# Kernel optimization log

Measured on AMD Instinct MI355X. Metric: run time of the kernel, lower is better.

## Reference

```python
import jax, jax.numpy as jnp
import numpy as np

N_NODES = 50000
N_EDGES = 800000
IN_DIM = 256
HID = 128
OUT = 128
LEAKY_SLOPE = 0.01


def setup_inputs() -> dict:
    key = jax.random.key(0)
    ks = jax.random.split(key, 12)
    s = 0.05
    return {
        "h": jax.random.normal(ks[0], (N_NODES, IN_DIM), dtype=jnp.float32),
        "src": jax.random.randint(ks[1], (N_EDGES,), 0, N_NODES, dtype=jnp.int32),
        "dst": jax.random.randint(ks[2], (N_EDGES,), 0, N_NODES, dtype=jnp.int32),
        "W1": jax.random.normal(ks[3], (HID, IN_DIM), dtype=jnp.float32) * s,
        "b1": jax.random.normal(ks[4], (HID,), dtype=jnp.float32) * s,
        "a1": jax.random.normal(ks[5], (2 * HID,), dtype=jnp.float32) * s,
        "ab1": jax.random.normal(ks[6], (), dtype=jnp.float32) * s,
        "W2": jax.random.normal(ks[7], (OUT, HID), dtype=jnp.float32) * s,
        "b2": jax.random.normal(ks[8], (OUT,), dtype=jnp.float32) * s,
        "a2": jax.random.normal(ks[9], (2 * OUT,), dtype=jnp.float32) * s,
        "ab2": jax.random.normal(ks[10], (), dtype=jnp.float32) * s,
    }


def gat_layer(h, src, dst, W, b, a, ab, n_nodes):
    # z = fc(h)
    z = h @ W.T + b                      # [N, D]
    D = z.shape[-1]
    zs = z[src]                           # [E, D] gather src features
    zd = z[dst]                           # [E, D] gather dst features
    # attn_fc(cat[zs, zd]) == zs @ a[:D] + zd @ a[D:] + ab
    e = zs @ a[:D] + zd @ a[D:] + ab      # [E]
    e = jnp.where(e > 0, e, LEAKY_SLOPE * e)  # leaky_relu, slope 0.01
    # segment softmax over edges grouped by destination node
    m = jax.ops.segment_max(e, dst, num_segments=n_nodes)   # [N]
    ex = jnp.exp(e - m[dst])                                  # [E]
    denom = jax.ops.segment_sum(ex, dst, num_segments=n_nodes)  # [N]
    alpha = ex / denom[dst]                                   # [E]
    # weighted scatter-sum of src features into dst nodes
    return jax.ops.segment_sum(alpha[:, None] * zs, dst, num_segments=n_nodes)


def reference(h, src, dst, W1, b1, a1, ab1, W2, b2, a2, ab2):
    n = h.shape[0]
    h1 = jax.nn.elu(gat_layer(h, src, dst, W1, b1, a1, ab1, n))
    h2 = jax.nn.elu(gat_layer(h1, src, dst, W2, b2, a2, ab2, n))
    return h2
```

## Files before the change

kernel.cpp:

```cpp
#include <hip/hip_runtime.h>
#include <hip/hip_bf16.h>

#define N_NODES 50000
#define N_EDGES 800000
#define IN_DIM  256
#define HID     128
#define LEAKY   0.01f

#define EDGE_BLOCKS  ((N_EDGES + 255) / 256)
#define NODE_WBLKS   (N_NODES / 4)
#define SCAN_BLOCKS  ((N_NODES + 255) / 256)
#define MTILES       ((N_NODES + 31) / 32)
#define GEMM_WAVES   (MTILES * 2)
#define GEMM_BLOCKS  ((GEMM_WAVES + 3) / 4)

typedef __attribute__((ext_vector_type(8))) short short8;
typedef __attribute__((ext_vector_type(4))) float f32x4;

__device__ __forceinline__ unsigned short f2bf(float x) {
    union { __hip_bfloat16 b; unsigned short u; } c;
    c.b = __float2bfloat16(x);
    return c.u;
}
__device__ __forceinline__ float bf2f(unsigned short u) {
    union { unsigned int u; float f; } c;
    c.u = ((unsigned int)u) << 16;
    return c.f;
}
__device__ __forceinline__ float2 bfu2(unsigned int u) {
    float2 r;
    r.x = bf2f((unsigned short)(u & 0xffff));
    r.y = bf2f((unsigned short)(u >> 16));
    return r;
}
__device__ __forceinline__ float lky(float x) { return x > 0.f ? x : LEAKY * x; }


__global__ void hist_split(const int* __restrict__ dst, int* __restrict__ counts,
                           const float* __restrict__ W1, unsigned short* __restrict__ w1hi,
                           unsigned short* __restrict__ w1lo,
                           const float* __restrict__ W2, unsigned short* __restrict__ w2hi,
                           unsigned short* __restrict__ w2lo) {
    int i = blockIdx.x * 256 + threadIdx.x;
    if (i < N_EDGES) atomicAdd(&counts[dst[i]], 1);
    if (i < HID * IN_DIM) {
        float x = W1[i];
        unsigned short h = f2bf(x);
        w1hi[i] = h;
        w1lo[i] = f2bf(x - bf2f(h));
    } else if (i < HID * IN_DIM + HID * HID) {
        int j = i - HID * IN_DIM;
        float x = W2[j];
        unsigned short h = f2bf(x);
        w2hi[j] = h;
        w2lo[j] = f2bf(x - bf2f(h));
    }
}

__global__ void scan_block(const int* __restrict__ counts, int* __restrict__ offsets,
                           int* __restrict__ bsums) {
    __shared__ int sh[256];
    int tid = threadIdx.x;
    int i = blockIdx.x * 256 + tid;
    int v = (i < N_NODES) ? counts[i] : 0;
    sh[tid] = v;
    __syncthreads();
    for (int o = 1; o < 256; o <<= 1) {
        int t = (tid >= o) ? sh[tid - o] : 0;
        __syncthreads();
        sh[tid] += t;
        __syncthreads();
    }
    if (i < N_NODES) offsets[i] = sh[tid] - v;
    if (tid == 255) bsums[blockIdx.x] = sh[255];
}

__global__ void scan_add(int* __restrict__ offsets, const int* __restrict__ bsums) {
    __shared__ int sh[256];
    int tid = threadIdx.x;
    int b = blockIdx.x;
    sh[tid] = (tid < b) ? bsums[tid] : 0;
    __syncthreads();
    for (int o = 128; o > 0; o >>= 1) {
        if (tid < o) sh[tid] += sh[tid + o];
        __syncthreads();
    }
    int base = sh[0];
    int i = b * 256 + tid;
    if (i < N_NODES) offsets[i] += base;
    if (i == N_NODES) offsets[N_NODES] = N_EDGES;
}

__global__ void fill_kernel(const int* __restrict__ dst, const int* __restrict__ src,
                            const int* __restrict__ offsets,
                            int* __restrict__ cursor, int* __restrict__ csr_src) {
    int i = blockIdx.x * 256 + threadIdx.x;
    if (i < N_EDGES) {
        int d = dst[i];
        int p = atomicAdd(&cursor[d], 1);
        csr_src[offsets[d] + p] = src[i];
    }
}


__device__ __forceinline__ void gemm_epilogue(
        const f32x4* acc, int m0, int q, int lane,
        const float* __restrict__ bias, const float* __restrict__ attn,
        unsigned short* __restrict__ Zb, float* __restrict__ sS, float* __restrict__ sD) {
    int r = lane & 15;
    int rowbase = m0 + (lane >> 4) * 4;
    float ps[4] = {0.f, 0.f, 0.f, 0.f};
    float pd[4] = {0.f, 0.f, 0.f, 0.f};
#pragma unroll
    for (int nt = 0; nt < 4; nt++) {
        int n = q * 64 + nt * 16 + r;
        float bn = bias[n];
        float aS = attn[n];
        float aD = attn[HID + n];
#pragma unroll
        for (int reg = 0; reg < 4; reg++) {
            float zv = acc[nt][reg] + bn;
            Zb[(size_t)(rowbase + reg) * HID + n] = f2bf(zv);
            ps[reg] += zv * aS;
            pd[reg] += zv * aD;
        }
    }
#pragma unroll
    for (int o = 1; o < 16; o <<= 1) {
#pragma unroll
        for (int reg = 0; reg < 4; reg++) {
            ps[reg] += __shfl_xor(ps[reg], o, 64);
            pd[reg] += __shfl_xor(pd[reg], o, 64);
        }
    }
    if (r == 0) {
#pragma unroll
        for (int reg = 0; reg < 4; reg++) {
            sS[q * N_NODES + rowbase + reg] = ps[reg];
            sD[q * N_NODES + rowbase + reg] = pd[reg];
        }
    }
}


__launch_bounds__(256)
__global__ void gemm_fc1(const float* __restrict__ A,
                         const unsigned short* __restrict__ Whi,
                         const unsigned short* __restrict__ Wlo,
                         const float* __restrict__ bias,
                         const float* __restrict__ attn,
                         unsigned short* __restrict__ Zb,
                         float* __restrict__ sS, float* __restrict__ sD) {
    int wave = blockIdx.x * 4 + (threadIdx.x >> 6);
    if (wave >= GEMM_WAVES) return;
    int lane = threadIdx.x & 63;
    int mt = wave >> 1;
    int q  = wave & 1;
    int m0 = mt * 32;
    bool has2 = (m0 + 16 < N_NODES);
    int r  = lane & 15;
    int ko = (lane >> 4) * 8;

    const float* Ap0 = A + (size_t)(m0 + r) * IN_DIM + ko;
    const float* Ap1 = has2 ? (Ap0 + 16 * IN_DIM) : Ap0;
    const unsigned short* Wh = Whi + (size_t)(q * 64 + r) * IN_DIM + ko;
    const unsigned short* Wl = Wlo + (size_t)(q * 64 + r) * IN_DIM + ko;

    f32x4 acc0[4], acc1[4];
#pragma unroll
    for (int i = 0; i < 4; i++) {
        acc0[i] = (f32x4){0.f, 0.f, 0.f, 0.f};
        acc1[i] = (f32x4){0.f, 0.f, 0.f, 0.f};
    }

    float4 c00 = *(const float4*)(Ap0);
    float4 c01 = *(const float4*)(Ap0 + 4);
    float4 c10 = *(const float4*)(Ap1);
    float4 c11 = *(const float4*)(Ap1 + 4);

#pragma unroll
    for (int kt = 0; kt < IN_DIM / 32; kt++) {
        float4 n00, n01, n10, n11;
        if (kt < IN_DIM / 32 - 1) {
            n00 = *(const float4*)(Ap0 + (kt + 1) * 32);
            n01 = *(const float4*)(Ap0 + (kt + 1) * 32 + 4);
            n10 = *(const float4*)(Ap1 + (kt + 1) * 32);
            n11 = *(const float4*)(Ap1 + (kt + 1) * 32 + 4);
        }
        float x0[8] = {c00.x, c00.y, c00.z, c00.w, c01.x, c01.y, c01.z, c01.w};
        float x1[8] = {c10.x, c10.y, c10.z, c10.w, c11.x, c11.y, c11.z, c11.w};
        short8 ahi0, alo0, ahi1, alo1;
#pragma unroll
        for (int j = 0; j < 8; j++) {
            unsigned short h0 = f2bf(x0[j]);
            ahi0[j] = (short)h0;
            alo0[j] = (short)f2bf(x0[j] - bf2f(h0));
            unsigned short h1 = f2bf(x1[j]);
            ahi1[j] = (short)h1;
            alo1[j] = (short)f2bf(x1[j] - bf2f(h1));
        }
#pragma unroll
        for (int nt = 0; nt < 4; nt++) {
            short8 bhi = *(const short8*)(Wh + (size_t)nt * 16 * IN_DIM + kt * 32);
            short8 blo = *(const short8*)(Wl + (size_t)nt * 16 * IN_DIM + kt * 32);
            acc0[nt] = __builtin_amdgcn_mfma_f32_16x16x32_bf16(ahi0, bhi, acc0[nt], 0, 0, 0);
            acc0[nt] = __builtin_amdgcn_mfma_f32_16x16x32_bf16(alo0, bhi, acc0[nt], 0, 0, 0);
            acc0[nt] = __builtin_amdgcn_mfma_f32_16x16x32_bf16(ahi0, blo, acc0[nt], 0, 0, 0);
            acc1[nt] = __builtin_amdgcn_mfma_f32_16x16x32_bf16(ahi1, bhi, acc1[nt], 0, 0, 0);
            acc1[nt] = __builtin_amdgcn_mfma_f32_16x16x32_bf16(alo1, bhi, acc1[nt], 0, 0, 0);
            acc1[nt] = __builtin_amdgcn_mfma_f32_16x16x32_bf16(ahi1, blo, acc1[nt], 0, 0, 0);
        }
        if (kt < IN_DIM / 32 - 1) { c00 = n00; c01 = n01; c10 = n10; c11 = n11; }
    }
    gemm_epilogue(acc0, m0, q, lane, bias, attn, Zb, sS, sD);
    if (has2) gemm_epilogue(acc1, m0 + 16, q, lane, bias, attn, Zb, sS, sD);
}


__launch_bounds__(256)
__global__ void gemm_fc2(const unsigned short* __restrict__ Abf,
                         const unsigned short* __restrict__ Whi,
                         const unsigned short* __restrict__ Wlo,
                         const float* __restrict__ bias,
                         const float* __restrict__ attn,
                         unsigned short* __restrict__ Zb,
                         float* __restrict__ sS, float* __restrict__ sD) {
    int wave = blockIdx.x * 4 + (threadIdx.x >> 6);
    if (wave >= GEMM_WAVES) return;
    int lane = threadIdx.x & 63;
    int mt = wave >> 1;
    int q  = wave & 1;
    int m0 = mt * 32;
    bool has2 = (m0 + 16 < N_NODES);
    int r  = lane & 15;
    int ko = (lane >> 4) * 8;

    const unsigned short* Ap0 = Abf + (size_t)(m0 + r) * HID + ko;
    const unsigned short* Ap1 = has2 ? (Ap0 + 16 * HID) : Ap0;
    const unsigned short* Wh = Whi + (size_t)(q * 64 + r) * HID + ko;
    const unsigned short* Wl = Wlo + (size_t)(q * 64 + r) * HID + ko;

    f32x4 acc0[4], acc1[4];
#pragma unroll
    for (int i = 0; i < 4; i++) {
        acc0[i] = (f32x4){0.f, 0.f, 0.f, 0.f};
        acc1[i] = (f32x4){0.f, 0.f, 0.f, 0.f};
    }

    short8 a0 = *(const short8*)(Ap0);
    short8 a1 = *(const short8*)(Ap1);

#pragma unroll
    for (int kt = 0; kt < HID / 32; kt++) {
        short8 na0, na1;
        if (kt < HID / 32 - 1) {
            na0 = *(const short8*)(Ap0 + (kt + 1) * 32);
            na1 = *(const short8*)(Ap1 + (kt + 1) * 32);
        }
#pragma unroll
        for (int nt = 0; nt < 4; nt++) {
            short8 bhi = *(const short8*)(Wh + (size_t)nt * 16 * HID + kt * 32);
            short8 blo = *(const short8*)(Wl + (size_t)nt * 16 * HID + kt * 32);
            acc0[nt] = __builtin_amdgcn_mfma_f32_16x16x32_bf16(a0, bhi, acc0[nt], 0, 0, 0);
            acc0[nt] = __builtin_amdgcn_mfma_f32_16x16x32_bf16(a0, blo, acc0[nt], 0, 0, 0);
            acc1[nt] = __builtin_amdgcn_mfma_f32_16x16x32_bf16(a1, bhi, acc1[nt], 0, 0, 0);
            acc1[nt] = __builtin_amdgcn_mfma_f32_16x16x32_bf16(a1, blo, acc1[nt], 0, 0, 0);
        }
        if (kt < HID / 32 - 1) { a0 = na0; a1 = na1; }
    }
    gemm_epilogue(acc0, m0, q, lane, bias, attn, Zb, sS, sD);
    if (has2) gemm_epilogue(acc1, m0 + 16, q, lane, bias, attn, Zb, sS, sD);
}


template <int OUT_BF>
__launch_bounds__(256)
__global__ void aggregate(const unsigned short* __restrict__ Zb,
                          const int* __restrict__ csr_src,
                          const int* __restrict__ offsets,
                          const float* __restrict__ sS,
                          const float* __restrict__ sD,
                          const float* __restrict__ ab,
                          unsigned short* __restrict__ OutBf,
                          float* __restrict__ OutF) {
    int v = blockIdx.x * 4 + (threadIdx.x >> 6);
    int lane = threadIdx.x & 63;
    int off = offsets[v];
    int deg = offsets[v + 1] - off;
    float sdv = sD[v] + sD[v + N_NODES] + ab[0];

    const unsigned int* Zrow = (const unsigned int*)Zb;
    float2 acc = {0.f, 0.f};

    if (deg <= 64) {
        bool act = lane < deg;
        int s_l = 0;
        float x = -3.0e38f;
        if (act) {
            s_l = csr_src[off + lane];
            x = lky(sS[s_l] + sS[s_l + N_NODES] + sdv);
        }
        float mx = x;
#pragma unroll
        for (int o = 32; o > 0; o >>= 1) mx = fmaxf(mx, __shfl_xor(mx, o, 64));
        float ex = act ? __expf(x - mx) : 0.f;
        float sum = ex;
#pragma unroll
        for (int o = 32; o > 0; o >>= 1) sum += __shfl_xor(sum, o, 64);
        float al_l = (deg > 0) ? ex / sum : 0.f;

        int t = 0;
        for (; t + 8 <= deg; t += 8) {
            int   s[8];
            float a[8];
            unsigned int rw[8];
#pragma unroll
            for (int j = 0; j < 8; j++) {
                s[j] = __shfl(s_l, t + j, 64);
                a[j] = __shfl(al_l, t + j, 64);
            }
#pragma unroll
            for (int j = 0; j < 8; j++)
                rw[j] = Zrow[(size_t)s[j] * (HID / 2) + lane];
#pragma unroll
            for (int j = 0; j < 8; j++) {
                float2 zz = bfu2(rw[j]);
                acc.x += a[j] * zz.x;
                acc.y += a[j] * zz.y;
            }
        }
        for (; t < deg; t++) {
            int sj = __shfl(s_l, t, 64);
            float aj = __shfl(al_l, t, 64);
            float2 zz = bfu2(Zrow[(size_t)sj * (HID / 2) + lane]);
            acc.x += aj * zz.x;
            acc.y += aj * zz.y;
        }
    } else {
        float mx = -3.0e38f;
        for (int t = lane; t < deg; t += 64) {
            int s = csr_src[off + t];
            mx = fmaxf(mx, lky(sS[s] + sS[s + N_NODES] + sdv));
        }
#pragma unroll
        for (int o = 32; o > 0; o >>= 1) mx = fmaxf(mx, __shfl_xor(mx, o, 64));
        float sum = 0.f;
        for (int t = lane; t < deg; t += 64) {
            int s = csr_src[off + t];
            sum += __expf(lky(sS[s] + sS[s + N_NODES] + sdv) - mx);
        }
#pragma unroll
        for (int o = 32; o > 0; o >>= 1) sum += __shfl_xor(sum, o, 64);
        float inv = 1.f / sum;
        for (int t = 0; t < deg; t++) {
            int s = csr_src[off + t];
            float al = __expf(lky(sS[s] + sS[s + N_NODES] + sdv) - mx) * inv;
            float2 zz = bfu2(Zrow[(size_t)s * (HID / 2) + lane]);
            acc.x += al * zz.x;
            acc.y += al * zz.y;
        }
    }

    acc.x = acc.x > 0.f ? acc.x : __expf(acc.x) - 1.f;
    acc.y = acc.y > 0.f ? acc.y : __expf(acc.y) - 1.f;

    if (OUT_BF) {
        ushort2 o2;
        o2.x = f2bf(acc.x);
        o2.y = f2bf(acc.y);
        *((ushort2*)(OutBf + (size_t)v * HID + lane * 2)) = o2;
    } else {
        float2 o2 = {acc.x, acc.y};
        *((float2*)(OutF + (size_t)v * HID + lane * 2)) = o2;
    }
}


extern "C" void kernel_launch(void* const* d_in, const int* in_sizes, int n_in,
                              void* d_out, int out_size, void* d_ws, size_t ws_size,
                              hipStream_t stream) {
    const float* h   = (const float*)d_in[0];
    const int*   src = (const int*)d_in[1];
    const int*   dst = (const int*)d_in[2];
    const float* W1  = (const float*)d_in[3];
    const float* b1  = (const float*)d_in[4];
    const float* a1  = (const float*)d_in[5];
    const float* ab1 = (const float*)d_in[6];
    const float* W2  = (const float*)d_in[7];
    const float* b2  = (const float*)d_in[8];
    const float* a2  = (const float*)d_in[9];
    const float* ab2 = (const float*)d_in[10];
    float* out = (float*)d_out;

    unsigned short* zb = (unsigned short*)d_ws;
    float* sS = (float*)(zb + (size_t)N_NODES * HID);
    float* sD = sS + 2 * N_NODES;
    int* counts  = (int*)(sD + 2 * N_NODES);
    int* cursor  = counts + N_NODES;
    int* offsets = cursor + N_NODES;
    int* bsums   = offsets + N_NODES + 16;
    unsigned short* h1   = (unsigned short*)(bsums + 256);
    unsigned short* w1hi = h1 + (size_t)N_NODES * HID;
    unsigned short* w1lo = w1hi + HID * IN_DIM;
    unsigned short* w2hi = w1lo + HID * IN_DIM;
    unsigned short* w2lo = w2hi + HID * HID;
    int* csr_src = (int*)(w2lo + HID * HID);

    hipMemsetAsync(counts, 0, 2 * (size_t)N_NODES * sizeof(int), stream);

    hist_split<<<EDGE_BLOCKS, 256, 0, stream>>>(dst, counts, W1, w1hi, w1lo, W2, w2hi, w2lo);
    scan_block<<<SCAN_BLOCKS, 256, 0, stream>>>(counts, offsets, bsums);
    scan_add<<<SCAN_BLOCKS, 256, 0, stream>>>(offsets, bsums);
    fill_kernel<<<EDGE_BLOCKS, 256, 0, stream>>>(dst, src, offsets, cursor, csr_src);

    gemm_fc1<<<GEMM_BLOCKS, 256, 0, stream>>>(h, w1hi, w1lo, b1, a1, zb, sS, sD);
    aggregate<1><<<NODE_WBLKS, 256, 0, stream>>>(zb, csr_src, offsets, sS, sD, ab1, h1, nullptr);

    gemm_fc2<<<GEMM_BLOCKS, 256, 0, stream>>>(h1, w2hi, w2lo, b2, a2, zb, sS, sD);
    aggregate<0><<<NODE_WBLKS, 256, 0, stream>>>(zb, csr_src, offsets, sS, sD, ab2, nullptr, out);
}
```

Before: 329.2 us.

## Presplit h into bf16 hi/lo in prep kernel and fuse CSR fill into fc1 GEMM

A prep kernel now converts the whole input h into bf16 hi/lo arrays, alongside the weight splitting and the dst histogram. The fc1 GEMM loads these pre-split operands instead of converting fp32 in its inner loop. The CSR fill step is folded into the fc1 GEMM launch as extra blocks, so it can overlap with the GEMM and one launch is saved. In exchange, h gets an extra full read-and-write pass through memory, while the GEMM reads the same number of bytes as before.

```diff
diff --git a/kernel.cpp b/kernel.cpp
--- a/kernel.cpp
+++ b/kernel.cpp
@@ -6,6 +6,11 @@
 #define IN_DIM  256
 #define HID     128
 #define LEAKY   0.01f
+
+#define H_ELEMS   (N_NODES * IN_DIM)
+#define W1_ELEMS  (HID * IN_DIM)
+#define W2_ELEMS  (HID * HID)
+#define PREP_BLOCKS ((H_ELEMS + W1_ELEMS + W2_ELEMS + N_EDGES) / 256)
 
 #define EDGE_BLOCKS  ((N_EDGES + 255) / 256)
 #define NODE_WBLKS   (N_NODES / 4)
@@ -13,6 +18,7 @@
 #define MTILES       ((N_NODES + 31) / 32)
 #define GEMM_WAVES   (MTILES * 2)
 #define GEMM_BLOCKS  ((GEMM_WAVES + 3) / 4)
+#define FC1_BLOCKS   (GEMM_BLOCKS + EDGE_BLOCKS)
 
 typedef __attribute__((ext_vector_type(8))) short short8;
 typedef __attribute__((ext_vector_type(4))) float f32x4;
@@ -36,25 +42,39 @@
 __device__ __forceinline__ float lky(float x) { return x > 0.f ? x : LEAKY * x; }
 
 
-__global__ void hist_split(const int* __restrict__ dst, int* __restrict__ counts,
-                           const float* __restrict__ W1, unsigned short* __restrict__ w1hi,
-                           unsigned short* __restrict__ w1lo,
-                           const float* __restrict__ W2, unsigned short* __restrict__ w2hi,
-                           unsigned short* __restrict__ w2lo) {
+__global__ void prep(const float* __restrict__ h,
+                     unsigned short* __restrict__ hhi, unsigned short* __restrict__ hlo,
+                     const float* __restrict__ W1, unsigned short* __restrict__ w1hi,
+                     unsigned short* __restrict__ w1lo,
+                     const float* __restrict__ W2, unsigned short* __restrict__ w2hi,
+                     unsigned short* __restrict__ w2lo,
+                     const int* __restrict__ dst, int* __restrict__ counts) {
     int i = blockIdx.x * 256 + threadIdx.x;
-    if (i < N_EDGES) atomicAdd(&counts[dst[i]], 1);
-    if (i < HID * IN_DIM) {
-        float x = W1[i];
-        unsigned short h = f2bf(x);
-        w1hi[i] = h;
-        w1lo[i] = f2bf(x - bf2f(h));
-    } else if (i < HID * IN_DIM + HID * HID) {
-        int j = i - HID * IN_DIM;
+    if (i < H_ELEMS) {
+        float x = h[i];
+        unsigned short hb = f2bf(x);
+        hhi[i] = hb;
+        hlo[i] = f2bf(x - bf2f(hb));
+        return;
+    }
+    int j = i - H_ELEMS;
+    if (j < W1_ELEMS) {
+        float x = W1[j];
+        unsigned short hb = f2bf(x);
+        w1hi[j] = hb;
+        w1lo[j] = f2bf(x - bf2f(hb));
+        return;
+    }
+    j -= W1_ELEMS;
+    if (j < W2_ELEMS) {
         float x = W2[j];
-        unsigned short h = f2bf(x);
-        w2hi[j] = h;
-        w2lo[j] = f2bf(x - bf2f(h));
-    }
+        unsigned short hb = f2bf(x);
+        w2hi[j] = hb;
+        w2lo[j] = f2bf(x - bf2f(hb));
+        return;
+    }
+    j -= W2_ELEMS;
+    atomicAdd(&counts[dst[j]], 1);
 }
 
 __global__ void scan_block(const int* __restrict__ counts, int* __restrict__ offsets,
@@ -91,17 +111,6 @@
     if (i == N_NODES) offsets[N_NODES] = N_EDGES;
 }
 
-__global__ void fill_kernel(const int* __restrict__ dst, const int* __restrict__ src,
-                            const int* __restrict__ offsets,
-                            int* __restrict__ cursor, int* __restrict__ csr_src) {
-    int i = blockIdx.x * 256 + threadIdx.x;
-    if (i < N_EDGES) {
-        int d = dst[i];
-        int p = atomicAdd(&cursor[d], 1);
-        csr_src[offsets[d] + p] = src[i];
-    }
-}
-
 
 __device__ __forceinline__ void gemm_epilogue(
         const f32x4* acc, int m0, int q, int lane,
@@ -144,13 +153,26 @@
 
 
 __launch_bounds__(256)
-__global__ void gemm_fc1(const float* __restrict__ A,
-                         const unsigned short* __restrict__ Whi,
-                         const unsigned short* __restrict__ Wlo,
-                         const float* __restrict__ bias,
-                         const float* __restrict__ attn,
-                         unsigned short* __restrict__ Zb,
-                         float* __restrict__ sS, float* __restrict__ sD) {
+__global__ void gemm_fc1_fill(const unsigned short* __restrict__ Ahi,
+                              const unsigned short* __restrict__ Alo,
+                              const unsigned short* __restrict__ Whi,
+                              const unsigned short* __restrict__ Wlo,
+                              const float* __restrict__ bias,
+                              const float* __restrict__ attn,
+                              unsigned short* __restrict__ Zb,
+                              float* __restrict__ sS, float* __restrict__ sD,
+                              const int* __restrict__ dst, const int* __restrict__ src,
+                              const int* __restrict__ offsets,
+                              int* __restrict__ cursor, int* __restrict__ csr_src) {
+    if (blockIdx.x >= GEMM_BLOCKS) {
+        int i = (blockIdx.x - GEMM_BLOCKS) * 256 + threadIdx.x;
+        if (i < N_EDGES) {
+            int d = dst[i];
+            int p = atomicAdd(&cursor[d], 1);
+            csr_src[offsets[d] + p] = src[i];
+        }
+        return;
+    }
     int wave = blockIdx.x * 4 + (threadIdx.x >> 6);
     if (wave >= GEMM_WAVES) return;
     int lane = threadIdx.x & 63;
@@ -161,8 +183,10 @@
     int r  = lane & 15;
     int ko = (lane >> 4) * 8;
 
-    const float* Ap0 = A + (size_t)(m0 + r) * IN_DIM + ko;
-    const float* Ap1 = has2 ? (Ap0 + 16 * IN_DIM) : Ap0;
+    const unsigned short* A0h = Ahi + (size_t)(m0 + r) * IN_DIM + ko;
+    const unsigned short* A0l = Alo + (size_t)(m0 + r) * IN_DIM + ko;
+    const unsigned short* A1h = has2 ? (A0h + 16 * IN_DIM) : A0h;
+    const unsigned short* A1l = has2 ? (A0l + 16 * IN_DIM) : A0l;
     const unsigned short* Wh = Whi + (size_t)(q * 64 + r) * IN_DIM + ko;
     const unsigned short* Wl = Wlo + (size_t)(q * 64 + r) * IN_DIM + ko;
 
@@ -173,44 +197,32 @@
         acc1[i] = (f32x4){0.f, 0.f, 0.f, 0.f};
     }
 
-    float4 c00 = *(const float4*)(Ap0);
-    float4 c01 = *(const float4*)(Ap0 + 4);
-    float4 c10 = *(const float4*)(Ap1);
-    float4 c11 = *(const float4*)(Ap1 + 4);
+    short8 a0h = *(const short8*)(A0h);
+    short8 a0l = *(const short8*)(A0l);
+    short8 a1h = *(const short8*)(A1h);
+    short8 a1l = *(const short8*)(A1l);
 
 #pragma unroll
     for (int kt = 0; kt < IN_DIM / 32; kt++) {
-        float4 n00, n01, n10, n11;
+        short8 n0h, n0l, n1h, n1l;
         if (kt < IN_DIM / 32 - 1) {
-            n00 = *(const float4*)(Ap0 + (kt + 1) * 32);
-            n01 = *(const float4*)(Ap0 + (kt + 1) * 32 + 4);
-            n10 = *(const float4*)(Ap1 + (kt + 1) * 32);
-            n11 = *(const float4*)(Ap1 + (kt + 1) * 32 + 4);
-        }
-        float x0[8] = {c00.x, c00.y, c00.z, c00.w, c01.x, c01.y, c01.z, c01.w};
-        float x1[8] = {c10.x, c10.y, c10.z, c10.w, c11.x, c11.y, c11.z, c11.w};
-        short8 ahi0, alo0, ahi1, alo1;
-#pragma unroll
-        for (int j = 0; j < 8; j++) {
-            unsigned short h0 = f2bf(x0[j]);
-            ahi0[j] = (short)h0;
-            alo0[j] = (short)f2bf(x0[j] - bf2f(h0));
-            unsigned short h1 = f2bf(x1[j]);
-            ahi1[j] = (short)h1;
-            alo1[j] = (short)f2bf(x1[j] - bf2f(h1));
+            n0h = *(const short8*)(A0h + (kt + 1) * 32);
+            n0l = *(const short8*)(A0l + (kt + 1) * 32);
+            n1h = *(const short8*)(A1h + (kt + 1) * 32);
+            n1l = *(const short8*)(A1l + (kt + 1) * 32);
         }
 #pragma unroll
         for (int nt = 0; nt < 4; nt++) {
             short8 bhi = *(const short8*)(Wh + (size_t)nt * 16 * IN_DIM + kt * 32);
             short8 blo = *(const short8*)(Wl + (size_t)nt * 16 * IN_DIM + kt * 32);
-            acc0[nt] = __builtin_amdgcn_mfma_f32_16x16x32_bf16(ahi0, bhi, acc0[nt], 0, 0, 0);
-            acc0[nt] = __builtin_amdgcn_mfma_f32_16x16x32_bf16(alo0, bhi, acc0[nt], 0, 0, 0);
-            acc0[nt] = __builtin_amdgcn_mfma_f32_16x16x32_bf16(ahi0, blo, acc0[nt], 0, 0, 0);
-            acc1[nt] = __builtin_amdgcn_mfma_f32_16x16x32_bf16(ahi1, bhi, acc1[nt], 0, 0, 0);
-            acc1[nt] = __builtin_amdgcn_mfma_f32_16x16x32_bf16(alo1, bhi, acc1[nt], 0, 0, 0);
-            acc1[nt] = __builtin_amdgcn_mfma_f32_16x16x32_bf16(ahi1, blo, acc1[nt], 0, 0, 0);
-        }
-        if (kt < IN_DIM / 32 - 1) { c00 = n00; c01 = n01; c10 = n10; c11 = n11; }
+            acc0[nt] = __builtin_amdgcn_mfma_f32_16x16x32_bf16(a0h, bhi, acc0[nt], 0, 0, 0);
+            acc0[nt] = __builtin_amdgcn_mfma_f32_16x16x32_bf16(a0l, bhi, acc0[nt], 0, 0, 0);
+            acc0[nt] = __builtin_amdgcn_mfma_f32_16x16x32_bf16(a0h, blo, acc0[nt], 0, 0, 0);
+            acc1[nt] = __builtin_amdgcn_mfma_f32_16x16x32_bf16(a1h, bhi, acc1[nt], 0, 0, 0);
+            acc1[nt] = __builtin_amdgcn_mfma_f32_16x16x32_bf16(a1l, bhi, acc1[nt], 0, 0, 0);
+            acc1[nt] = __builtin_amdgcn_mfma_f32_16x16x32_bf16(a1h, blo, acc1[nt], 0, 0, 0);
+        }
+        if (kt < IN_DIM / 32 - 1) { a0h = n0h; a0l = n0l; a1h = n1h; a1l = n1l; }
     }
     gemm_epilogue(acc0, m0, q, lane, bias, attn, Zb, sS, sD);
     if (has2) gemm_epilogue(acc1, m0 + 16, q, lane, bias, attn, Zb, sS, sD);
@@ -401,19 +413,23 @@
     int* bsums   = offsets + N_NODES + 16;
     unsigned short* h1   = (unsigned short*)(bsums + 256);
     unsigned short* w1hi = h1 + (size_t)N_NODES * HID;
-    unsigned short* w1lo = w1hi + HID * IN_DIM;
-    unsigned short* w2hi = w1lo + HID * IN_DIM;
-    unsigned short* w2lo = w2hi + HID * HID;
-    int* csr_src = (int*)(w2lo + HID * HID);
+    unsigned short* w1lo = w1hi + W1_ELEMS;
+    unsigned short* w2hi = w1lo + W1_ELEMS;
+    unsigned short* w2lo = w2hi + W2_ELEMS;
+    int* csr_src = (int*)(w2lo + W2_ELEMS);
+    unsigned short* hhi = (unsigned short*)(csr_src + N_EDGES);
+    unsigned short* hlo = hhi + (size_t)H_ELEMS;
 
     hipMemsetAsync(counts, 0, 2 * (size_t)N_NODES * sizeof(int), stream);
 
-    hist_split<<<EDGE_BLOCKS, 256, 0, stream>>>(dst, counts, W1, w1hi, w1lo, W2, w2hi, w2lo);
+    prep<<<PREP_BLOCKS, 256, 0, stream>>>(h, hhi, hlo, W1, w1hi, w1lo,
+                                          W2, w2hi, w2lo, dst, counts);
     scan_block<<<SCAN_BLOCKS, 256, 0, stream>>>(counts, offsets, bsums);
     scan_add<<<SCAN_BLOCKS, 256, 0, stream>>>(offsets, bsums);
-    fill_kernel<<<EDGE_BLOCKS, 256, 0, stream>>>(dst, src, offsets, cursor, csr_src);
-
-    gemm_fc1<<<GEMM_BLOCKS, 256, 0, stream>>>(h, w1hi, w1lo, b1, a1, zb, sS, sD);
+
+    gemm_fc1_fill<<<FC1_BLOCKS, 256, 0, stream>>>(hhi, hlo, w1hi, w1lo, b1, a1,
+                                                  zb, sS, sD,
+                                                  dst, src, offsets, cursor, csr_src);
     aggregate<1><<<NODE_WBLKS, 256, 0, stream>>>(zb, csr_src, offsets, sS, sD, ab1, h1, nullptr);
 
     gemm_fc2<<<GEMM_BLOCKS, 256, 0, stream>>>(h1, w2hi, w2lo, b2, a2, zb, sS, sD);
```

Result: slower. 341.2 us (+3.6%).

## Stage GEMM tiles through LDS with 96-row blocks and shared bf16 splits

Applied to the files above, without the earlier changes.

Both FC GEMMs now load a 96-row A tile and the full weight tile into shared memory per 64-wide K chunk. Four waves split the tile by row half and column half. Previously each wave streamed A and the hi/lo weights straight from global memory, converted A to hi/lo bf16 itself, and reread the same weights in every wave. The new layout converts A once per block, reuses it across both column halves, and cuts redundant weight traffic, at the cost of more LDS use, barriers, and bounds checks for the ragged last block.

```diff
diff --git a/kernel.cpp b/kernel.cpp
--- a/kernel.cpp
+++ b/kernel.cpp
@@ -10,9 +10,12 @@
 #define EDGE_BLOCKS  ((N_EDGES + 255) / 256)
 #define NODE_WBLKS   (N_NODES / 4)
 #define SCAN_BLOCKS  ((N_NODES + 255) / 256)
-#define MTILES       ((N_NODES + 31) / 32)
-#define GEMM_WAVES   (MTILES * 2)
-#define GEMM_BLOCKS  ((GEMM_WAVES + 3) / 4)
+#define W1_ELEMS  (HID * IN_DIM)
+#define W2_ELEMS  (HID * HID)
+
+#define TM        96
+#define FC_BLOCKS ((N_NODES + TM - 1) / TM)
+#define LDA       72
 
 typedef __attribute__((ext_vector_type(8))) short short8;
 typedef __attribute__((ext_vector_type(4))) float f32x4;
@@ -43,13 +46,13 @@
                            unsigned short* __restrict__ w2lo) {
     int i = blockIdx.x * 256 + threadIdx.x;
     if (i < N_EDGES) atomicAdd(&counts[dst[i]], 1);
-    if (i < HID * IN_DIM) {
+    if (i < W1_ELEMS) {
         float x = W1[i];
         unsigned short h = f2bf(x);
         w1hi[i] = h;
         w1lo[i] = f2bf(x - bf2f(h));
-    } else if (i < HID * IN_DIM + HID * HID) {
-        int j = i - HID * IN_DIM;
+    } else if (i < W1_ELEMS + W2_ELEMS) {
+        int j = i - W1_ELEMS;
         float x = W2[j];
         unsigned short h = f2bf(x);
         w2hi[j] = h;
@@ -103,12 +106,13 @@
 }
 
 
-__device__ __forceinline__ void gemm_epilogue(
-        const f32x4* acc, int m0, int q, int lane,
-        const float* __restrict__ bias, const float* __restrict__ attn,
-        unsigned short* __restrict__ Zb, float* __restrict__ sS, float* __restrict__ sD) {
+__device__ __forceinline__ void epi(const f32x4* accn, int mbase, int q, int lane,
+                                    const float* __restrict__ bias,
+                                    const float* __restrict__ attn,
+                                    unsigned short* __restrict__ Zb,
+                                    float* __restrict__ sS, float* __restrict__ sD) {
     int r = lane & 15;
-    int rowbase = m0 + (lane >> 4) * 4;
+    int rowbase = mbase + (lane >> 4) * 4;
     float ps[4] = {0.f, 0.f, 0.f, 0.f};
     float pd[4] = {0.f, 0.f, 0.f, 0.f};
 #pragma unroll
@@ -119,8 +123,9 @@
         float aD = attn[HID + n];
 #pragma unroll
         for (int reg = 0; reg < 4; reg++) {
-            float zv = acc[nt][reg] + bn;
-            Zb[(size_t)(rowbase + reg) * HID + n] = f2bf(zv);
+            float zv = accn[nt][reg] + bn;
+            if (rowbase + reg < N_NODES)
+                Zb[(size_t)(rowbase + reg) * HID + n] = f2bf(zv);
             ps[reg] += zv * aS;
             pd[reg] += zv * aD;
         }
@@ -136,8 +141,10 @@
     if (r == 0) {
 #pragma unroll
         for (int reg = 0; reg < 4; reg++) {
-            sS[q * N_NODES + rowbase + reg] = ps[reg];
-            sD[q * N_NODES + rowbase + reg] = pd[reg];
+            if (rowbase + reg < N_NODES) {
+                sS[q * N_NODES + rowbase + reg] = ps[reg];
+                sD[q * N_NODES + rowbase + reg] = pd[reg];
+            }
         }
     }
 }
@@ -151,69 +158,82 @@
                          const float* __restrict__ attn,
                          unsigned short* __restrict__ Zb,
                          float* __restrict__ sS, float* __restrict__ sD) {
-    int wave = blockIdx.x * 4 + (threadIdx.x >> 6);
-    if (wave >= GEMM_WAVES) return;
-    int lane = threadIdx.x & 63;
-    int mt = wave >> 1;
-    int q  = wave & 1;
-    int m0 = mt * 32;
-    bool has2 = (m0 + 16 < N_NODES);
-    int r  = lane & 15;
-    int ko = (lane >> 4) * 8;
-
-    const float* Ap0 = A + (size_t)(m0 + r) * IN_DIM + ko;
-    const float* Ap1 = has2 ? (Ap0 + 16 * IN_DIM) : Ap0;
-    const unsigned short* Wh = Whi + (size_t)(q * 64 + r) * IN_DIM + ko;
-    const unsigned short* Wl = Wlo + (size_t)(q * 64 + r) * IN_DIM + ko;
-
-    f32x4 acc0[4], acc1[4];
-#pragma unroll
-    for (int i = 0; i < 4; i++) {
-        acc0[i] = (f32x4){0.f, 0.f, 0.f, 0.f};
-        acc1[i] = (f32x4){0.f, 0.f, 0.f, 0.f};
-    }
-
-    float4 c00 = *(const float4*)(Ap0);
-    float4 c01 = *(const float4*)(Ap0 + 4);
-    float4 c10 = *(const float4*)(Ap1);
-    float4 c11 = *(const float4*)(Ap1 + 4);
-
-#pragma unroll
-    for (int kt = 0; kt < IN_DIM / 32; kt++) {
-        float4 n00, n01, n10, n11;
-        if (kt < IN_DIM / 32 - 1) {
-            n00 = *(const float4*)(Ap0 + (kt + 1) * 32);
-            n01 = *(const float4*)(Ap0 + (kt + 1) * 32 + 4);
-            n10 = *(const float4*)(Ap1 + (kt + 1) * 32);
-            n11 = *(const float4*)(Ap1 + (kt + 1) * 32 + 4);
-        }
-        float x0[8] = {c00.x, c00.y, c00.z, c00.w, c01.x, c01.y, c01.z, c01.w};
-        float x1[8] = {c10.x, c10.y, c10.z, c10.w, c11.x, c11.y, c11.z, c11.w};
-        short8 ahi0, alo0, ahi1, alo1;
-#pragma unroll
-        for (int j = 0; j < 8; j++) {
-            unsigned short h0 = f2bf(x0[j]);
-            ahi0[j] = (short)h0;
-            alo0[j] = (short)f2bf(x0[j] - bf2f(h0));
-            unsigned short h1 = f2bf(x1[j]);
-            ahi1[j] = (short)h1;
-            alo1[j] = (short)f2bf(x1[j] - bf2f(h1));
-        }
-#pragma unroll
-        for (int nt = 0; nt < 4; nt++) {
-            short8 bhi = *(const short8*)(Wh + (size_t)nt * 16 * IN_DIM + kt * 32);
-            short8 blo = *(const short8*)(Wl + (size_t)nt * 16 * IN_DIM + kt * 32);
-            acc0[nt] = __builtin_amdgcn_mfma_f32_16x16x32_bf16(ahi0, bhi, acc0[nt], 0, 0, 0);
-            acc0[nt] = __builtin_amdgcn_mfma_f32_16x16x32_bf16(alo0, bhi, acc0[nt], 0, 0, 0);
-            acc0[nt] = __builtin_amdgcn_mfma_f32_16x16x32_bf16(ahi0, blo, acc0[nt], 0, 0, 0);
-            acc1[nt] = __builtin_amdgcn_mfma_f32_16x16x32_bf16(ahi1, bhi, acc1[nt], 0, 0, 0);
-            acc1[nt] = __builtin_amdgcn_mfma_f32_16x16x32_bf16(alo1, bhi, acc1[nt], 0, 0, 0);
-            acc1[nt] = __builtin_amdgcn_mfma_f32_16x16x32_bf16(ahi1, blo, acc1[nt], 0, 0, 0);
-        }
-        if (kt < IN_DIM / 32 - 1) { c00 = n00; c01 = n01; c10 = n10; c11 = n11; }
-    }
-    gemm_epilogue(acc0, m0, q, lane, bias, attn, Zb, sS, sD);
-    if (has2) gemm_epilogue(acc1, m0 + 16, q, lane, bias, attn, Zb, sS, sD);
+    __shared__ unsigned short Ah[TM * LDA];
+    __shared__ unsigned short Al[TM * LDA];
+    __shared__ unsigned short Bh[HID * LDA];
+    __shared__ unsigned short Bl[HID * LDA];
+
+    int tid  = threadIdx.x;
+    int lane = tid & 63;
+    int w    = tid >> 6;
+    int q    = w & 1;
+    int mh   = w >> 1;
+    int m0   = blockIdx.x * TM;
+    int r    = lane & 15;
+    int koff = (lane >> 4) * 8;
+
+    f32x4 acc[3][4];
+#pragma unroll
+    for (int s = 0; s < 3; s++)
+#pragma unroll
+        for (int nt = 0; nt < 4; nt++) acc[s][nt] = (f32x4){0.f, 0.f, 0.f, 0.f};
+
+    for (int kc = 0; kc < IN_DIM / 64; kc++) {
+        int k0 = kc * 64;
+        __syncthreads();
+#pragma unroll
+        for (int j = 0; j < 6; j++) {
+            int flat = j * 256 + tid;
+            int row = flat >> 4;
+            int c4 = (flat & 15) << 2;
+            int gr = m0 + row;
+            if (gr >= N_NODES) gr = N_NODES - 1;
+            float4 v = *(const float4*)(A + (size_t)gr * IN_DIM + k0 + c4);
+            unsigned short h0 = f2bf(v.x), h1 = f2bf(v.y), h2 = f2bf(v.z), h3 = f2bf(v.w);
+            short4 hv = {(short)h0, (short)h1, (short)h2, (short)h3};
+            short4 lv = {(short)f2bf(v.x - bf2f(h0)), (short)f2bf(v.y - bf2f(h1)),
+                         (short)f2bf(v.z - bf2f(h2)), (short)f2bf(v.w - bf2f(h3))};
+            *(short4*)&Ah[row * LDA + c4] = hv;
+            *(short4*)&Al[row * LDA + c4] = lv;
+        }
+#pragma unroll
+        for (int j = 0; j < 4; j++) {
+            int flat = j * 256 + tid;
+            int n = flat >> 3;
+            int c8 = (flat & 7) << 3;
+            *(short8*)&Bh[n * LDA + c8] = *(const short8*)(Whi + (size_t)n * IN_DIM + k0 + c8);
+            *(short8*)&Bl[n * LDA + c8] = *(const short8*)(Wlo + (size_t)n * IN_DIM + k0 + c8);
+        }
+        __syncthreads();
+#pragma unroll
+        for (int ks = 0; ks < 2; ks++) {
+            int kk = ks * 32 + koff;
+            short8 ah[3], al[3], bh[4], bl[4];
+#pragma unroll
+            for (int s = 0; s < 3; s++) {
+                int row = mh * 48 + s * 16 + r;
+                ah[s] = *(const short8*)&Ah[row * LDA + kk];
+                al[s] = *(const short8*)&Al[row * LDA + kk];
+            }
+#pragma unroll
+            for (int nt = 0; nt < 4; nt++) {
+                int n = q * 64 + nt * 16 + r;
+                bh[nt] = *(const short8*)&Bh[n * LDA + kk];
+                bl[nt] = *(const short8*)&Bl[n * LDA + kk];
+            }
+#pragma unroll
+            for (int s = 0; s < 3; s++)
+#pragma unroll
+                for (int nt = 0; nt < 4; nt++) {
+                    acc[s][nt] = __builtin_amdgcn_mfma_f32_16x16x32_bf16(ah[s], bh[nt], acc[s][nt], 0, 0, 0);
+                    acc[s][nt] = __builtin_amdgcn_mfma_f32_16x16x32_bf16(al[s], bh[nt], acc[s][nt], 0, 0, 0);
+                    acc[s][nt] = __builtin_amdgcn_mfma_f32_16x16x32_bf16(ah[s], bl[nt], acc[s][nt], 0, 0, 0);
+                }
+        }
+    }
+#pragma unroll
+    for (int s = 0; s < 3; s++)
+        epi(acc[s], m0 + mh * 48 + s * 16, q, lane, bias, attn, Zb, sS, sD);
 }
 
 
@@ -225,51 +245,73 @@
                          const float* __restrict__ attn,
                          unsigned short* __restrict__ Zb,
                          float* __restrict__ sS, float* __restrict__ sD) {
-    int wave = blockIdx.x * 4 + (threadIdx.x >> 6);
-    if (wave >= GEMM_WAVES) return;
-    int lane = threadIdx.x & 63;
-    int mt = wave >> 1;
-    int q  = wave & 1;
-    int m0 = mt * 32;
-    bool has2 = (m0 + 16 < N_NODES);
-    int r  = lane & 15;
-    int ko = (lane >> 4) * 8;
-
-    const unsigned short* Ap0 = Abf + (size_t)(m0 + r) * HID + ko;
-    const unsigned short* Ap1 = has2 ? (Ap0 + 16 * HID) : Ap0;
-    const unsigned short* Wh = Whi + (size_t)(q * 64 + r) * HID + ko;
-    const unsigned short* Wl = Wlo + (size_t)(q * 64 + r) * HID + ko;
-
-    f32x4 acc0[4], acc1[4];
-#pragma unroll
-    for (int i = 0; i < 4; i++) {
-        acc0[i] = (f32x4){0.f, 0.f, 0.f, 0.f};
-        acc1[i] = (f32x4){0.f, 0.f, 0.f, 0.f};
-    }
-
-    short8 a0 = *(const short8*)(Ap0);
-    short8 a1 = *(const short8*)(Ap1);
-
-#pragma unroll
-    for (int kt = 0; kt < HID / 32; kt++) {
-        short8 na0, na1;
-        if (kt < HID / 32 - 1) {
-            na0 = *(const short8*)(Ap0 + (kt + 1) * 32);
-            na1 = *(const short8*)(Ap1 + (kt + 1) * 32);
-        }
-#pragma unroll
-        for (int nt = 0; nt < 4; nt++) {
-            short8 bhi = *(const short8*)(Wh + (size_t)nt * 16 * HID + kt * 32);
-            short8 blo = *(const short8*)(Wl + (size_t)nt * 16 * HID + kt * 32);
-            acc0[nt] = __builtin_amdgcn_mfma_f32_16x16x32_bf16(a0, bhi, acc0[nt], 0, 0, 0);
-            acc0[nt] = __builtin_amdgcn_mfma_f32_16x16x32_bf16(a0, blo, acc0[nt], 0, 0, 0);
-            acc1[nt] = __builtin_amdgcn_mfma_f32_16x16x32_bf16(a1, bhi, acc1[nt], 0, 0, 0);
-            acc1[nt] = __builtin_amdgcn_mfma_f32_16x16x32_bf16(a1, blo, acc1[nt], 0, 0, 0);
-        }
-        if (kt < HID / 32 - 1) { a0 = na0; a1 = na1; }
-    }
-    gemm_epilogue(acc0, m0, q, lane, bias, attn, Zb, sS, sD);
-    if (has2) gemm_epilogue(acc1, m0 + 16, q, lane, bias, attn, Zb, sS, sD);
+    __shared__ unsigned short Ah[TM * LDA];
+    __shared__ unsigned short Bh[HID * LDA];
+    __shared__ unsigned short Bl[HID * LDA];
+
+    int tid  = threadIdx.x;
+    int lane = tid & 63;
+    int w    = tid >> 6;
+    int q    = w & 1;
+    int mh   = w >> 1;
+    int m0   = blockIdx.x * TM;
+    int r    = lane & 15;
+    int koff = (lane >> 4) * 8;
+
+    f32x4 acc[3][4];
+#pragma unroll
+    for (int s = 0; s < 3; s++)
+#pragma unroll
+        for (int nt = 0; nt < 4; nt++) acc[s][nt] = (f32x4){0.f, 0.f, 0.f, 0.f};
+
+    for (int kc = 0; kc < HID / 64; kc++) {
+        int k0 = kc * 64;
+        __syncthreads();
+#pragma unroll
+        for (int j = 0; j < 3; j++) {
+            int flat = j * 256 + tid;
+            int row = flat >> 3;
+            int c8 = (flat & 7) << 3;
+            int gr = m0 + row;
+            if (gr >= N_NODES) gr = N_NODES - 1;
+            *(short8*)&Ah[row * LDA + c8] = *(const short8*)(Abf + (size_t)gr * HID + k0 + c8);
+        }
+#pragma unroll
+        for (int j = 0; j < 4; j++) {
+            int flat = j * 256 + tid;
+            int n = flat >> 3;
+            int c8 = (flat & 7) << 3;
+            *(short8*)&Bh[n * LDA + c8] = *(const short8*)(Whi + (size_t)n * HID + k0 + c8);
+            *(short8*)&Bl[n * LDA + c8] = *(const short8*)(Wlo + (size_t)n * HID + k0 + c8);
+        }
+        __syncthreads();
+#pragma unroll
+        for (int ks = 0; ks < 2; ks++) {
+            int kk = ks * 32 + koff;
+            short8 ah[3], bh[4], bl[4];
+#pragma unroll
+            for (int s = 0; s < 3; s++) {
+                int row = mh * 48 + s * 16 + r;
+                ah[s] = *(const short8*)&Ah[row * LDA + kk];
+            }
+#pragma unroll
+            for (int nt = 0; nt < 4; nt++) {
+                int n = q * 64 + nt * 16 + r;
+                bh[nt] = *(const short8*)&Bh[n * LDA + kk];
+                bl[nt] = *(const short8*)&Bl[n * LDA + kk];
+            }
+#pragma unroll
+            for (int s = 0; s < 3; s++)
+#pragma unroll
+                for (int nt = 0; nt < 4; nt++) {
+                    acc[s][nt] = __builtin_amdgcn_mfma_f32_16x16x32_bf16(ah[s], bh[nt], acc[s][nt], 0, 0, 0);
+                    acc[s][nt] = __builtin_amdgcn_mfma_f32_16x16x32_bf16(ah[s], bl[nt], acc[s][nt], 0, 0, 0);
+                }
+        }
+    }
+#pragma unroll
+    for (int s = 0; s < 3; s++)
+        epi(acc[s], m0 + mh * 48 + s * 16, q, lane, bias, attn, Zb, sS, sD);
 }
 
 
@@ -401,10 +443,10 @@
     int* bsums   = offsets + N_NODES + 16;
     unsigned short* h1   = (unsigned short*)(bsums + 256);
     unsigned short* w1hi = h1 + (size_t)N_NODES * HID;
-    unsigned short* w1lo = w1hi + HID * IN_DIM;
-    unsigned short* w2hi = w1lo + HID * IN_DIM;
-    unsigned short* w2lo = w2hi + HID * HID;
-    int* csr_src = (int*)(w2lo + HID * HID);
+    unsigned short* w1lo = w1hi + W1_ELEMS;
+    unsigned short* w2hi = w1lo + W1_ELEMS;
+    unsigned short* w2lo = w2hi + W2_ELEMS;
+    int* csr_src = (int*)(w2lo + W2_ELEMS);
 
     hipMemsetAsync(counts, 0, 2 * (size_t)N_NODES * sizeof(int), stream);
 
@@ -413,9 +455,9 @@
     scan_add<<<SCAN_BLOCKS, 256, 0, stream>>>(offsets, bsums);
     fill_kernel<<<EDGE_BLOCKS, 256, 0, stream>>>(dst, src, offsets, cursor, csr_src);
 
-    gemm_fc1<<<GEMM_BLOCKS, 256, 0, stream>>>(h, w1hi, w1lo, b1, a1, zb, sS, sD);
+    gemm_fc1<<<FC_BLOCKS, 256, 0, stream>>>(h, w1hi, w1lo, b1, a1, zb, sS, sD);
     aggregate<1><<<NODE_WBLKS, 256, 0, stream>>>(zb, csr_src, offsets, sS, sD, ab1, h1, nullptr);
 
-    gemm_fc2<<<GEMM_BLOCKS, 256, 0, stream>>>(h1, w2hi, w2lo, b2, a2, zb, sS, sD);
+    gemm_fc2<<<FC_BLOCKS, 256, 0, stream>>>(h1, w2hi, w2lo, b2, a2, zb, sS, sD);
     aggregate<0><<<NODE_WBLKS, 256, 0, stream>>>(zb, csr_src, offsets, sS, sD, ab2, nullptr, out);
 }
```

Result: faster. 303.7 us (-7.7%).
